# Performance work log

Hardware: AMD Instinct MI355X
Metric: run time of the kernel (lower is better)

Reference implementation:

```python
import jax, jax.numpy as jnp
import numpy as np

N_STUDENT = 100000
N_ITEM = 20000
N_EDGES = 1000000
IN_CH = 128
EDGE_DIM = 32
DEC_CH = 64


def setup_inputs() -> dict:
    key = jax.random.key(0)
    ks = jax.random.split(key, 9)
    x_student = jax.random.normal(ks[0], (N_STUDENT, IN_CH), dtype=jnp.float32)
    x_item = jax.random.normal(ks[1], (N_ITEM, IN_CH), dtype=jnp.float32)
    edge_label_index = jax.random.randint(ks[2], (2, N_EDGES), 0, N_ITEM, dtype=jnp.int64)
    edge_feat = jax.random.normal(ks[3], (N_EDGES, EDGE_DIM), dtype=jnp.float32)
    offset = jax.random.normal(ks[4], (N_ITEM, 1), dtype=jnp.float32)
    # linear: (IN_CH + EDGE_DIM) -> DEC_CH ; linear_2: IN_CH -> DEC_CH
    s1 = 1.0 / np.sqrt(IN_CH + EDGE_DIM)
    s2 = 1.0 / np.sqrt(IN_CH)
    W1 = jax.random.uniform(ks[5], (IN_CH + EDGE_DIM, DEC_CH), minval=-s1, maxval=s1, dtype=jnp.float32)
    b1 = jax.random.uniform(ks[6], (DEC_CH,), minval=-s1, maxval=s1, dtype=jnp.float32)
    W2 = jax.random.uniform(ks[7], (IN_CH, DEC_CH), minval=-s2, maxval=s2, dtype=jnp.float32)
    b2 = jax.random.uniform(ks[8], (DEC_CH,), minval=-s2, maxval=s2, dtype=jnp.float32)
    return {
        "x_student": x_student, "x_item": x_item,
        "edge_label_index": edge_label_index, "edge_feat": edge_feat,
        "offset": offset, "W1": W1, "b1": b1, "W2": W2, "b2": b2,
    }


def reference(x_student, x_item, edge_label_index, edge_feat, offset, W1, b1, W2, b2):
    # Gather edge endpoints: [E, IN_CH]
    feat_s = x_student[edge_label_index[0]]
    feat_i = x_item[edge_label_index[1]]
    # x = elu(Linear(cat([feat_s, edge_feat])))  -> [E, DEC_CH]
    x = jnp.concatenate([feat_s, edge_feat], axis=-1)
    x = jax.nn.elu(x @ W1 + b1)
    # y = softplus(Linear_2(feat_i))  -> [E, DEC_CH]
    y = jax.nn.softplus(feat_i @ W2 + b2)
    # elementwise mult + sum reduce -> [E, 1]
    out = jnp.sum(x * y, axis=-1, keepdims=True)
    # offset gather by item index, add
    out = out + offset[edge_label_index[1]]
    return out
```

## Files before the change

### kernel.cpp

```cpp
#include <hip/hip_runtime.h>
#include <math.h>

#define N_STUDENT 100000
#define N_ITEM    20000
#define N_EDGES   1000000
#define IN_CH     128
#define EDGE_DIM  32
#define DEC_CH    64

#define N_ROWS    N_ITEM


typedef __attribute__((ext_vector_type(8))) short short8;
typedef __attribute__((ext_vector_type(4))) float f32x4;

__device__ __forceinline__ short bf16_rne(float f) {
    union { float f; unsigned u; } v; v.f = f;
    unsigned r = (v.u + 0x7FFFu + ((v.u >> 16) & 1u)) >> 16;
    return (short)r;
}

__device__ __forceinline__ short8 cvt8(f32x4 a0, f32x4 a1) {
    short8 s;
    s[0] = bf16_rne(a0[0]); s[1] = bf16_rne(a0[1]);
    s[2] = bf16_rne(a0[2]); s[3] = bf16_rne(a0[3]);
    s[4] = bf16_rne(a1[0]); s[5] = bf16_rne(a1[1]);
    s[6] = bf16_rne(a1[2]); s[7] = bf16_rne(a1[3]);
    return s;
}

__device__ __forceinline__ float bf2f(unsigned short u) {
    union { unsigned u; float f; } v; v.u = ((unsigned)u) << 16;
    return v.f;
}

#define PRE_BLOCKS 1250

__global__ __launch_bounds__(64) void precompute_kernel(
    const float* __restrict__ x_student, const float* __restrict__ x_item,
    const float* __restrict__ W1, const float* __restrict__ b1,
    const float* __restrict__ W2, const float* __restrict__ b2,
    unsigned short* __restrict__ s_part, unsigned short* __restrict__ y_item)
{
    const int phase = (blockIdx.x >= PRE_BLOCKS);
    const int blk   = phase ? blockIdx.x - PRE_BLOCKS : blockIdx.x;
    const float* X  = phase ? x_item : x_student;
    const float* W  = phase ? W2 : W1;
    const float* B  = phase ? b2 : b1;
    unsigned short* OUT = phase ? y_item : s_part;

    const int lane = threadIdx.x;
    const int m = lane & 15, q = lane >> 4;
    const int r0w = blk * 16;

    short8 bfr[4][4];
    #pragma unroll
    for (int ks = 0; ks < 4; ++ks)
        #pragma unroll
        for (int ct = 0; ct < 4; ++ct)
            #pragma unroll
            for (int j = 0; j < 8; ++j)
                bfr[ks][ct][j] = bf16_rne(W[(ks * 32 + q * 8 + j) * DEC_CH + ct * 16 + m]);

    float bc[4];
    #pragma unroll
    for (int ct = 0; ct < 4; ++ct) bc[ct] = B[ct * 16 + m];

    const float* xp = X + (size_t)(r0w + m) * IN_CH + q * 8;

    f32x4 acc[4];
    #pragma unroll
    for (int ct = 0; ct < 4; ++ct) acc[ct] = (f32x4){bc[ct], bc[ct], bc[ct], bc[ct]};

    #pragma unroll
    for (int ks = 0; ks < 4; ++ks) {
        f32x4 a0 = *(const f32x4*)(xp + ks * 32);
        f32x4 a1 = *(const f32x4*)(xp + ks * 32 + 4);
        short8 af = cvt8(a0, a1);
        #pragma unroll
        for (int ct = 0; ct < 4; ++ct)
            acc[ct] = __builtin_amdgcn_mfma_f32_16x16x32_bf16(af, bfr[ks][ct], acc[ct], 0, 0, 0);
    }

    #pragma unroll
    for (int reg = 0; reg < 4; ++reg) {
        const int orow = r0w + q * 4 + reg;
        float f0, f1, f2, f3;
        if (phase) {
            f0 = fmaxf(acc[0][reg], 0.f) + log1pf(__expf(-fabsf(acc[0][reg])));
            f1 = fmaxf(acc[1][reg], 0.f) + log1pf(__expf(-fabsf(acc[1][reg])));
            f2 = fmaxf(acc[2][reg], 0.f) + log1pf(__expf(-fabsf(acc[2][reg])));
            f3 = fmaxf(acc[3][reg], 0.f) + log1pf(__expf(-fabsf(acc[3][reg])));
        } else {
            f0 = acc[0][reg]; f1 = acc[1][reg];
            f2 = acc[2][reg]; f3 = acc[3][reg];
        }
        ushort4 sv;
        sv.x = (unsigned short)bf16_rne(f0);
        sv.y = (unsigned short)bf16_rne(f1);
        sv.z = (unsigned short)bf16_rne(f2);
        sv.w = (unsigned short)bf16_rne(f3);
        *(ushort4*)(OUT + (size_t)orow * DEC_CH + m * 4) = sv;
    }
}

__global__ __launch_bounds__(256, 4) void edge_kernel(
    const int* __restrict__ idx, const float* __restrict__ ef,
    const float* __restrict__ W1, const float* __restrict__ offset,
    const unsigned short* __restrict__ s_part, const unsigned short* __restrict__ y_item,
    float* __restrict__ out)
{
    __shared__ int2  sIdx[256];
    __shared__ float sOff[256];

    const int lane = threadIdx.x & 63;
    const int m = lane & 15, q = lane >> 4;
    const int e0 = blockIdx.x * 256;
    const int wib = threadIdx.x >> 6;
    const int ew0 = e0 + wib * 64;

    {
        const int t = threadIdx.x;
        const int e = min(e0 + t, N_EDGES - 1);
        const int is = __builtin_nontemporal_load(idx + e);
        const int ii = __builtin_nontemporal_load(idx + N_EDGES + e);
        sIdx[t] = make_int2(is, ii);
        sOff[t] = offset[ii];
    }

    f32x4 a0[4], a1[4];
    #pragma unroll
    for (int rt = 0; rt < 4; ++rt) {
        const int er = min(ew0 + rt * 16 + m, N_EDGES - 1);
        const float* ap = ef + (size_t)er * EDGE_DIM + q * 8;
        a0[rt] = __builtin_nontemporal_load((const f32x4*)ap);
        a1[rt] = __builtin_nontemporal_load((const f32x4*)(ap + 4));
    }
    short8 af[4];
    #pragma unroll
    for (int rt = 0; rt < 4; ++rt) af[rt] = cvt8(a0[rt], a1[rt]);

    const float* Wb = W1 + IN_CH * DEC_CH;
    short8 bfr[4];
    #pragma unroll
    for (int ct = 0; ct < 4; ++ct)
        #pragma unroll
        for (int j = 0; j < 8; ++j)
            bfr[ct][j] = bf16_rne(Wb[(q * 8 + j) * DEC_CH + ct * 16 + m]);

    __syncthreads();

    ushort4 sg[4][4], yg[4][4];
    #pragma unroll
    for (int rt = 0; rt < 4; ++rt) {
        #pragma unroll
        for (int r = 0; r < 4; ++r) {
            const int2 ip = sIdx[wib * 64 + rt * 16 + q * 4 + r];
            sg[rt][r] = *(const ushort4*)(s_part + (size_t)ip.x * DEC_CH + m * 4);
            yg[rt][r] = *(const ushort4*)(y_item + (size_t)ip.y * DEC_CH + m * 4);
        }
    }

    const bool live = (ew0 < N_EDGES);

    #pragma unroll
    for (int rt = 0; rt < 4; ++rt) {
        f32x4 acc[4];
        #pragma unroll
        for (int ct = 0; ct < 4; ++ct) {
            f32x4 z = {0.f, 0.f, 0.f, 0.f};
            acc[ct] = __builtin_amdgcn_mfma_f32_16x16x32_bf16(af[rt], bfr[ct], z, 0, 0, 0);
        }

        float pr[4];
        #pragma unroll
        for (int r = 0; r < 4; ++r) {
            float t0 = acc[0][r] + bf2f(sg[rt][r].x);
            float t1 = acc[1][r] + bf2f(sg[rt][r].y);
            float t2 = acc[2][r] + bf2f(sg[rt][r].z);
            float t3 = acc[3][r] + bf2f(sg[rt][r].w);
            float x0 = t0 > 0.f ? t0 : (__expf(t0) - 1.f);
            float x1 = t1 > 0.f ? t1 : (__expf(t1) - 1.f);
            float x2 = t2 > 0.f ? t2 : (__expf(t2) - 1.f);
            float x3 = t3 > 0.f ? t3 : (__expf(t3) - 1.f);
            float p = x0 * bf2f(yg[rt][r].x);
            p = fmaf(x1, bf2f(yg[rt][r].y), p);
            p = fmaf(x2, bf2f(yg[rt][r].z), p);
            p = fmaf(x3, bf2f(yg[rt][r].w), p);
            pr[r] = p;
        }

        #pragma unroll
        for (int s = 1; s <= 8; s <<= 1) {
            pr[0] += __shfl_xor(pr[0], s, 64);
            pr[1] += __shfl_xor(pr[1], s, 64);
            pr[2] += __shfl_xor(pr[2], s, 64);
            pr[3] += __shfl_xor(pr[3], s, 64);
        }

        float v = (m & 3) == 0 ? pr[0]
                : (m & 3) == 1 ? pr[1]
                : (m & 3) == 2 ? pr[2] : pr[3];
        if (live && m < 4) {
            const int el = wib * 64 + rt * 16 + q * 4 + m;
            __builtin_nontemporal_store(v + sOff[el], &out[e0 + el]);
        }
    }
}

extern "C" void kernel_launch(void* const* d_in, const int* in_sizes, int n_in,
                              void* d_out, int out_size, void* d_ws, size_t ws_size,
                              hipStream_t stream) {
    const float* x_student = (const float*)d_in[0];
    const float* x_item    = (const float*)d_in[1];
    const int*   eli       = (const int*)d_in[2];
    const float* edge_feat = (const float*)d_in[3];
    const float* offset    = (const float*)d_in[4];
    const float* W1        = (const float*)d_in[5];
    const float* b1        = (const float*)d_in[6];
    const float* W2        = (const float*)d_in[7];
    const float* b2        = (const float*)d_in[8];
    float* out = (float*)d_out;

    unsigned short* s_part = (unsigned short*)d_ws;
    unsigned short* y_item = s_part + (size_t)N_ROWS * DEC_CH;

    precompute_kernel<<<2 * PRE_BLOCKS, 64, 0, stream>>>(
        x_student, x_item, W1, b1, W2, b2, s_part, y_item);
    edge_kernel<<<(N_EDGES + 255) / 256, 256, 0, stream>>>(
        eli, edge_feat, W1, offset, s_part, y_item, out);
}
```

Baseline: 258.8 us.

## Convert edge kernel to persistent grid-stride loop with double-buffered prefetch

The edge kernel now launches a fixed 512 blocks, and each wave loops over 64-edge chunks with a grid stride. Two register sets (A and B) ping-pong: the index loads, edge-feature loads and gathers for the next chunk are issued before the current chunk is computed, so memory latency overlaps with MFMA and ELU work. Indices and offsets are broadcast with wave shuffles instead of shared memory, which removes the block barrier. The doubled register state may lower occupancy, and the occupancy hint was dropped from the launch bounds.

```diff
diff --git a/kernel.cpp b/kernel.cpp
--- a/kernel.cpp
+++ b/kernel.cpp
@@ -104,41 +104,85 @@
     }
 }
 
-__global__ __launch_bounds__(256, 4) void edge_kernel(
+#define EDGE_BLOCKS 512
+#define NWAVES (EDGE_BLOCKS * 4)
+#define NCHUNK (N_EDGES / 64)
+
+#define IDX_LOAD(S, cb) { \
+    S##_eb = (cb) * 64; \
+    S##_is = __builtin_nontemporal_load(idx + S##_eb + lane); \
+    S##_ii = __builtin_nontemporal_load(idx + N_EDGES + S##_eb + lane); }
+
+#define EF_LOAD(S) { \
+    _Pragma("unroll") \
+    for (int rt = 0; rt < 4; ++rt) { \
+        const float* ap = ef + (size_t)(S##_eb + rt * 16 + m) * EDGE_DIM + q * 8; \
+        S##_a0[rt] = __builtin_nontemporal_load((const f32x4*)ap); \
+        S##_a1[rt] = __builtin_nontemporal_load((const f32x4*)(ap + 4)); } }
+
+#define GATH(S) { \
+    S##_off = offset[S##_ii]; \
+    _Pragma("unroll") \
+    for (int rt = 0; rt < 4; ++rt) { \
+        _Pragma("unroll") \
+        for (int r = 0; r < 4; ++r) { \
+            const int sl = rt * 16 + q * 4 + r; \
+            const int sis = __shfl(S##_is, sl, 64); \
+            const int sii = __shfl(S##_ii, sl, 64); \
+            S##_sg[rt][r] = *(const ushort4*)(s_part + (size_t)sis * DEC_CH + m * 4); \
+            S##_yg[rt][r] = *(const ushort4*)(y_item + (size_t)sii * DEC_CH + m * 4); } } }
+
+#define CVT_AF(S) { \
+    _Pragma("unroll") \
+    for (int rt = 0; rt < 4; ++rt) S##_af[rt] = cvt8(S##_a0[rt], S##_a1[rt]); }
+
+#define COMPUTE_STORE(S, EB) { \
+    _Pragma("unroll") \
+    for (int rt = 0; rt < 4; ++rt) { \
+        f32x4 acc[4]; \
+        _Pragma("unroll") \
+        for (int ct = 0; ct < 4; ++ct) { \
+            f32x4 z = {0.f, 0.f, 0.f, 0.f}; \
+            acc[ct] = __builtin_amdgcn_mfma_f32_16x16x32_bf16(S##_af[rt], bfr[ct], z, 0, 0, 0); } \
+        float pr[4]; \
+        _Pragma("unroll") \
+        for (int r = 0; r < 4; ++r) { \
+            float t0 = acc[0][r] + bf2f(S##_sg[rt][r].x); \
+            float t1 = acc[1][r] + bf2f(S##_sg[rt][r].y); \
+            float t2 = acc[2][r] + bf2f(S##_sg[rt][r].z); \
+            float t3 = acc[3][r] + bf2f(S##_sg[rt][r].w); \
+            float x0 = t0 > 0.f ? t0 : (__expf(t0) - 1.f); \
+            float x1 = t1 > 0.f ? t1 : (__expf(t1) - 1.f); \
+            float x2 = t2 > 0.f ? t2 : (__expf(t2) - 1.f); \
+            float x3 = t3 > 0.f ? t3 : (__expf(t3) - 1.f); \
+            float p = x0 * bf2f(S##_yg[rt][r].x); \
+            p = fmaf(x1, bf2f(S##_yg[rt][r].y), p); \
+            p = fmaf(x2, bf2f(S##_yg[rt][r].z), p); \
+            p = fmaf(x3, bf2f(S##_yg[rt][r].w), p); \
+            pr[r] = p; } \
+        _Pragma("unroll") \
+        for (int s = 1; s <= 8; s <<= 1) { \
+            pr[0] += __shfl_xor(pr[0], s, 64); \
+            pr[1] += __shfl_xor(pr[1], s, 64); \
+            pr[2] += __shfl_xor(pr[2], s, 64); \
+            pr[3] += __shfl_xor(pr[3], s, 64); } \
+        float v = (m & 3) == 0 ? pr[0] \
+                : (m & 3) == 1 ? pr[1] \
+                : (m & 3) == 2 ? pr[2] : pr[3]; \
+        const float offv = __shfl(S##_off, rt * 16 + q * 4 + m, 64); \
+        if (m < 4) \
+            __builtin_nontemporal_store(v + offv, &out[(EB) + rt * 16 + q * 4 + m]); \
+    } }
+
+__global__ __launch_bounds__(256) void edge_kernel(
     const int* __restrict__ idx, const float* __restrict__ ef,
     const float* __restrict__ W1, const float* __restrict__ offset,
     const unsigned short* __restrict__ s_part, const unsigned short* __restrict__ y_item,
     float* __restrict__ out)
 {
-    __shared__ int2  sIdx[256];
-    __shared__ float sOff[256];
-
     const int lane = threadIdx.x & 63;
     const int m = lane & 15, q = lane >> 4;
-    const int e0 = blockIdx.x * 256;
-    const int wib = threadIdx.x >> 6;
-    const int ew0 = e0 + wib * 64;
-
-    {
-        const int t = threadIdx.x;
-        const int e = min(e0 + t, N_EDGES - 1);
-        const int is = __builtin_nontemporal_load(idx + e);
-        const int ii = __builtin_nontemporal_load(idx + N_EDGES + e);
-        sIdx[t] = make_int2(is, ii);
-        sOff[t] = offset[ii];
-    }
-
-    f32x4 a0[4], a1[4];
-    #pragma unroll
-    for (int rt = 0; rt < 4; ++rt) {
-        const int er = min(ew0 + rt * 16 + m, N_EDGES - 1);
-        const float* ap = ef + (size_t)er * EDGE_DIM + q * 8;
-        a0[rt] = __builtin_nontemporal_load((const f32x4*)ap);
-        a1[rt] = __builtin_nontemporal_load((const f32x4*)(ap + 4));
-    }
-    short8 af[4];
-    #pragma unroll
-    for (int rt = 0; rt < 4; ++rt) af[rt] = cvt8(a0[rt], a1[rt]);
+    const int wgid = blockIdx.x * 4 + (threadIdx.x >> 6);
 
     const float* Wb = W1 + IN_CH * DEC_CH;
     short8 bfr[4];
@@ -148,63 +192,43 @@
         for (int j = 0; j < 8; ++j)
             bfr[ct][j] = bf16_rne(Wb[(q * 8 + j) * DEC_CH + ct * 16 + m]);
 
-    __syncthreads();
-
-    ushort4 sg[4][4], yg[4][4];
-    #pragma unroll
-    for (int rt = 0; rt < 4; ++rt) {
-        #pragma unroll
-        for (int r = 0; r < 4; ++r) {
-            const int2 ip = sIdx[wib * 64 + rt * 16 + q * 4 + r];
-            sg[rt][r] = *(const ushort4*)(s_part + (size_t)ip.x * DEC_CH + m * 4);
-            yg[rt][r] = *(const ushort4*)(y_item + (size_t)ip.y * DEC_CH + m * 4);
-        }
-    }
-
-    const bool live = (ew0 < N_EDGES);
-
-    #pragma unroll
-    for (int rt = 0; rt < 4; ++rt) {
-        f32x4 acc[4];
-        #pragma unroll
-        for (int ct = 0; ct < 4; ++ct) {
-            f32x4 z = {0.f, 0.f, 0.f, 0.f};
-            acc[ct] = __builtin_amdgcn_mfma_f32_16x16x32_bf16(af[rt], bfr[ct], z, 0, 0, 0);
-        }
-
-        float pr[4];
-        #pragma unroll
-        for (int r = 0; r < 4; ++r) {
-            float t0 = acc[0][r] + bf2f(sg[rt][r].x);
-            float t1 = acc[1][r] + bf2f(sg[rt][r].y);
-            float t2 = acc[2][r] + bf2f(sg[rt][r].z);
-            float t3 = acc[3][r] + bf2f(sg[rt][r].w);
-            float x0 = t0 > 0.f ? t0 : (__expf(t0) - 1.f);
-            float x1 = t1 > 0.f ? t1 : (__expf(t1) - 1.f);
-            float x2 = t2 > 0.f ? t2 : (__expf(t2) - 1.f);
-            float x3 = t3 > 0.f ? t3 : (__expf(t3) - 1.f);
-            float p = x0 * bf2f(yg[rt][r].x);
-            p = fmaf(x1, bf2f(yg[rt][r].y), p);
-            p = fmaf(x2, bf2f(yg[rt][r].z), p);
-            p = fmaf(x3, bf2f(yg[rt][r].w), p);
-            pr[r] = p;
-        }
-
-        #pragma unroll
-        for (int s = 1; s <= 8; s <<= 1) {
-            pr[0] += __shfl_xor(pr[0], s, 64);
-            pr[1] += __shfl_xor(pr[1], s, 64);
-            pr[2] += __shfl_xor(pr[2], s, 64);
-            pr[3] += __shfl_xor(pr[3], s, 64);
-        }
-
-        float v = (m & 3) == 0 ? pr[0]
-                : (m & 3) == 1 ? pr[1]
-                : (m & 3) == 2 ? pr[2] : pr[3];
-        if (live && m < 4) {
-            const int el = wib * 64 + rt * 16 + q * 4 + m;
-            __builtin_nontemporal_store(v + sOff[el], &out[e0 + el]);
-        }
+    int A_eb, A_is, A_ii;  float A_off;
+    int B_eb, B_is, B_ii;  float B_off;
+    f32x4 A_a0[4], A_a1[4], B_a0[4], B_a1[4];
+    short8 A_af[4], B_af[4];
+    ushort4 A_sg[4][4], A_yg[4][4], B_sg[4][4], B_yg[4][4];
+
+    int cA = wgid;
+    IDX_LOAD(A, cA);
+    int cB = cA + NWAVES;
+    bool haveB = (cB < NCHUNK);
+    if (haveB) IDX_LOAD(B, cB);
+    EF_LOAD(A);
+    GATH(A);
+    CVT_AF(A);
+    int cN = cB + NWAVES;
+
+    while (true) {
+        if (!haveB) { COMPUTE_STORE(A, A_eb); return; }
+        EF_LOAD(B);
+        GATH(B);
+        const bool haveN = (cN < NCHUNK);
+        const int ebA = A_eb;
+        if (haveN) IDX_LOAD(A, cN);
+        COMPUTE_STORE(A, ebA);
+        CVT_AF(B);
+
+        if (!haveN) { COMPUTE_STORE(B, B_eb); return; }
+        EF_LOAD(A);
+        GATH(A);
+        const bool haveN2 = (cN + NWAVES < NCHUNK);
+        const int ebB = B_eb;
+        if (haveN2) IDX_LOAD(B, cN + NWAVES);
+        COMPUTE_STORE(B, ebB);
+        CVT_AF(A);
+
+        haveB = haveN2;
+        cN += 2 * NWAVES;
     }
 }
 
@@ -227,6 +251,6 @@
 
     precompute_kernel<<<2 * PRE_BLOCKS, 64, 0, stream>>>(
         x_student, x_item, W1, b1, W2, b2, s_part, y_item);
-    edge_kernel<<<(N_EDGES + 255) / 256, 256, 0, stream>>>(
+    edge_kernel<<<EDGE_BLOCKS, 256, 0, stream>>>(
         eli, edge_feat, W1, offset, s_part, y_item, out);
 }
```

Result: slower. 295.2 us (+14.1%).
